# Kernel optimization log

Hardware: AMD Instinct MI355X
Metric: run time of the kernel (lower is better)

Reference implementation:

```python
import jax, jax.numpy as jnp
import numpy as np

DIM = 1024
NUM_HEADS = 16
NUM_KV_HEADS = 4
HEAD_DIM = DIM // NUM_HEADS  # 64
GROUP = NUM_HEADS // NUM_KV_HEADS  # 4
SCALE = HEAD_DIM ** -0.5


def setup_inputs() -> dict:
    key = jax.random.key(0)
    ks = jax.random.split(key, 6)
    B, N = 2, 2048
    x = jax.random.normal(ks[0], (B, N, DIM), dtype=jnp.float32)
    s = DIM ** -0.5
    Wq = jax.random.normal(ks[1], (DIM, DIM), dtype=jnp.float32) * s
    Wk = jax.random.normal(ks[2], (DIM, NUM_KV_HEADS * HEAD_DIM), dtype=jnp.float32) * s
    Wv = jax.random.normal(ks[3], (DIM, NUM_KV_HEADS * HEAD_DIM), dtype=jnp.float32) * s
    Wo = jax.random.normal(ks[4], (DIM, DIM), dtype=jnp.float32) * s
    bo = jax.random.normal(ks[5], (DIM,), dtype=jnp.float32) * 0.01
    return {"x": x, "Wq": Wq, "Wk": Wk, "Wv": Wv, "Wo": Wo, "bo": bo}


def reference(x, Wq, Wk, Wv, Wo, bo):
    B, N, C = x.shape
    # projections
    q = (x @ Wq).reshape(B, N, NUM_HEADS, HEAD_DIM)          # B N H D
    k = (x @ Wk).reshape(B, N, NUM_KV_HEADS, HEAD_DIM)       # B N Kh D
    v = (x @ Wv).reshape(B, N, NUM_KV_HEADS, HEAD_DIM)
    # group query heads: H = Kh * GROUP; broadcast KV per group (no repeat copy)
    q = q.reshape(B, N, NUM_KV_HEADS, GROUP, HEAD_DIM)
    # scores: B Kh G Nq Nk
    attn = jnp.einsum('bqhgd,bkhd->bhgqk', q, k) * SCALE
    attn = jax.nn.softmax(attn, axis=-1)
    out = jnp.einsum('bhgqk,bkhd->bqhgd', attn, v)           # B N Kh G D
    out = out.reshape(B, N, C)
    return out @ Wo + bo
```

## Files before the change

### kernel.cpp

```cpp
#include <hip/hip_runtime.h>
#include <hip/hip_bf16.h>


typedef unsigned short u16;
typedef short s8 __attribute__((ext_vector_type(8)));
typedef float f4 __attribute__((ext_vector_type(4)));
typedef u16 u16x8 __attribute__((ext_vector_type(8)));

__device__ __forceinline__ unsigned pk2(float a, float b) {
  __hip_bfloat162 h = __float22bfloat162_rn(make_float2(a, b));
  unsigned u; __builtin_memcpy(&u, &h, 4); return u;
}
__device__ __forceinline__ u16 bf1(float a) {
  __hip_bfloat16 h = __float2bfloat16(a);
  u16 u; __builtin_memcpy(&u, &h, 2); return u;
}
__device__ __forceinline__ float ex2(float x) {
#if __has_builtin(__builtin_amdgcn_exp2f)
  return __builtin_amdgcn_exp2f(x);
#else
  return exp2f(x);
#endif
}
__device__ __forceinline__ void glds16(const u16* g, u16* l) {
  __builtin_amdgcn_global_load_lds((const __attribute__((address_space(1))) unsigned*)g,
                                   (__attribute__((address_space(3))) unsigned*)l, 16, 0, 0);
}

__global__ __launch_bounds__(256) void cvt_x(const float* __restrict__ x, u16* __restrict__ xb) {
  const int n4 = (4096 * 1024) / 4;
  for (int i = blockIdx.x * 256 + threadIdx.x; i < n4; i += gridDim.x * 256) {
    float4 f = ((const float4*)x)[i];
    uint2 o; o.x = pk2(f.x, f.y); o.y = pk2(f.z, f.w);
    ((uint2*)xb)[i] = o;
  }
}

__global__ __launch_bounds__(256) void cvt_w(const float* __restrict__ Wq, const float* __restrict__ Wk,
                                             const float* __restrict__ Wv, const float* __restrict__ Wo,
                                             u16* __restrict__ wqkvt, u16* __restrict__ wot) {
  __shared__ u16 T[64][68];
  const int m = blockIdx.z;
  const float* src; u16* dst; int N; int drow0; float scale;
  if (m == 0)      { src = Wq; N = 1024; dst = wqkvt; drow0 = 0;    scale = 0.18033688011112042f; }
  else if (m == 1) { src = Wk; N = 256;  dst = wqkvt; drow0 = 1024; scale = 1.f; }
  else if (m == 2) { src = Wv; N = 256;  dst = wqkvt; drow0 = 1280; scale = 1.f; }
  else             { src = Wo; N = 1024; dst = wot;   drow0 = 0;    scale = 1.f; }
  const int n0 = blockIdx.x * 64, k0 = blockIdx.y * 64;
  if (n0 >= N) return;
  const int tid = threadIdx.x;
  const int rr = tid >> 4, cc = (tid & 15) * 4;
#pragma unroll
  for (int it = 0; it < 4; ++it) {
    const int r = rr + it * 16;
    float4 f = *(const float4*)&src[(k0 + r) * N + n0 + cc];
    uint2 o; o.x = pk2(f.x * scale, f.y * scale); o.y = pk2(f.z * scale, f.w * scale);
    *(uint2*)&T[r][cc] = o;
  }
  __syncthreads();
  const int nn = tid >> 3, kq = (tid & 7) * 8;
#pragma unroll
  for (int it = 0; it < 2; ++it) {
    const int n = nn + it * 32;
    u16x8 v;
#pragma unroll
    for (int j = 0; j < 8; ++j) v[j] = T[kq + j][n];
    *(u16x8*)&dst[(drow0 + n0 + n) * 1024 + k0 + kq] = v;
  }
}

__global__ __launch_bounds__(256) void vtrans(const u16* __restrict__ vc, u16* __restrict__ vt) {
  __shared__ u16 T[64][72];
  const int tok0 = blockIdx.x * 64, d0 = blockIdx.y * 64, b = blockIdx.z;
  const int tid = threadIdx.x;
  const int r = tid >> 3, cc = (tid & 7) * 8;
#pragma unroll
  for (int it = 0; it < 2; ++it) {
    const int row = r + it * 32;
    *(u16x8*)&T[row][cc] = *(const u16x8*)&vc[(b * 2048 + tok0 + row) * 256 + d0 + cc];
  }
  __syncthreads();
#pragma unroll
  for (int it = 0; it < 2; ++it) {
    const int d = (tid >> 3) + it * 32;
    const int gd = d0 + d, kh = gd >> 6, dd = gd & 63;
    u16x8 v;
#pragma unroll
    for (int j = 0; j < 8; ++j) v[j] = T[(tid & 7) * 8 + j][d];
    *(u16x8*)&vt[((b * 4 + kh) * 64 + dd) * 2048 + tok0 + (tid & 7) * 8] = v;
  }
}

template<int MODE>
__global__ __launch_bounds__(256) void gemm_bt(const u16* __restrict__ A, const u16* __restrict__ Bt,
                                               u16* __restrict__ Cq, u16* __restrict__ Vc,
                                               float* __restrict__ Cf, const float* __restrict__ bias,
                                               const int K) {
  __shared__ u16 As[128 * 32];
  __shared__ u16 Bs[128 * 32];
  const int tid = threadIdx.x, lane = tid & 63, w = tid >> 6;
  const int wm = w >> 1, wn = w & 1;
  const int m0 = blockIdx.y * 128, n0 = blockIdx.x * 128;
  const int g = lane >> 4, c = lane & 15;
  const int srow = w * 32 + (lane >> 2), scol = (lane & 3) * 8;
  const u16* ga = A + (m0 + srow) * K + scol;
  const u16* gb = Bt + (n0 + srow) * K + scol;
  f4 acc[4][4] = {};
  for (int k0 = 0; k0 < K; k0 += 32) {
    glds16(ga,           &As[w * 1024]);
    glds16(ga + 16 * K,  &As[w * 1024 + 512]);
    glds16(gb,           &Bs[w * 1024]);
    glds16(gb + 16 * K,  &Bs[w * 1024 + 512]);
    ga += 32; gb += 32;
    __syncthreads();
    s8 a[4], b[4];
#pragma unroll
    for (int m = 0; m < 4; ++m) a[m] = *(const s8*)&As[(wm * 64 + m * 16 + c) * 32 + g * 8];
#pragma unroll
    for (int n = 0; n < 4; ++n) b[n] = *(const s8*)&Bs[(wn * 64 + n * 16 + c) * 32 + g * 8];
    __builtin_amdgcn_s_setprio(1);
#pragma unroll
    for (int m = 0; m < 4; ++m)
#pragma unroll
      for (int n = 0; n < 4; ++n)
        acc[m][n] = __builtin_amdgcn_mfma_f32_16x16x32_bf16(a[m], b[n], acc[m][n], 0, 0, 0);
    __builtin_amdgcn_s_setprio(0);
    __syncthreads();
  }
#pragma unroll
  for (int m = 0; m < 4; ++m) {
#pragma unroll
    for (int n = 0; n < 4; ++n) {
#pragma unroll
      for (int r = 0; r < 4; ++r) {
        const int row = m0 + wm * 64 + m * 16 + g * 4 + r;
        const int col = n0 + wn * 64 + n * 16 + c;
        if (MODE == 0) {
          const u16 hv = bf1(acc[m][n][r]);
          if (col < 1280) Cq[row * 1280 + col] = hv;
          else            Vc[row * 256 + (col - 1280)] = hv;
        } else {
          Cf[row * 1024 + col] = acc[m][n][r] + bias[col];
        }
      }
    }
  }
}

__global__ __launch_bounds__(256) void attn_fwd(const u16* __restrict__ qkv, const u16* __restrict__ vt,
                                                u16* __restrict__ ao) {
  __shared__ u16 QP[64 * 64];
  __shared__ u16 Ks[2][64 * 64];
  __shared__ u16 Vs[2][64 * 64];
  const int tid = threadIdx.x, lane = tid & 63, w = tid >> 6;
  const int h = blockIdx.y, b = blockIdx.z, kh = h >> 2;
  const int q0 = blockIdx.x * 64;
  const int g = lane >> 4, c = lane & 15;
  const int srow = w * 16 + (lane >> 3), sch = lane & 7;

#pragma unroll
  for (int j = 0; j < 2; ++j) {
    const int qq = srow + j * 8;
    const int d0 = (sch ^ (qq & 7)) << 3;
    glds16(qkv + (b * 2048 + q0 + qq) * 1280 + h * 64 + d0, &QP[w * 1024 + j * 512]);
  }
  const int rr0 = srow, rr1 = srow + 8;
  const u16* kg0 = qkv + ((b * 2048 + rr0) * 1280) + 1024 + kh * 64 + ((sch ^ (rr0 & 7)) << 3);
  const u16* kg1 = qkv + ((b * 2048 + rr1) * 1280) + 1024 + kh * 64 + ((sch ^ (rr1 & 7)) << 3);
  const u16* vg0 = vt + ((b * 4 + kh) * 64 + rr0) * 2048 + ((sch ^ (rr0 & 7)) << 3);
  const u16* vg1 = vt + ((b * 4 + kh) * 64 + rr1) * 2048 + ((sch ^ (rr1 & 7)) << 3);
  glds16(kg0, &Ks[0][w * 1024]); glds16(kg1, &Ks[0][w * 1024 + 512]);
  glds16(vg0, &Vs[0][w * 1024]); glds16(vg1, &Vs[0][w * 1024 + 512]);
  __syncthreads();

  s8 qf[2];
  {
    const int q = w * 16 + c;
    qf[0] = *(const s8*)&QP[q * 64 + (((0 + g) ^ (q & 7)) << 3)];
    qf[1] = *(const s8*)&QP[q * 64 + (((4 + g) ^ (q & 7)) << 3)];
  }
  const int kb0 = c * 64 + (((0 + g) ^ (c & 7)) << 3);
  const int kb1 = c * 64 + (((4 + g) ^ (c & 7)) << 3);
  const int pwbase = w * 1024 + c * 64;

  s8 ones;
#pragma unroll
  for (int j = 0; j < 8; ++j) ones[j] = (short)0x3F80;

  f4 acc[4] = {};
  f4 accS = {};
  int cur = 0;

  for (int kt = 0; kt < 32; ++kt) {
    if (kt < 31) {
      kg0 += 64 * 1280; kg1 += 64 * 1280; vg0 += 64; vg1 += 64;
      glds16(kg0, &Ks[cur ^ 1][w * 1024]); glds16(kg1, &Ks[cur ^ 1][w * 1024 + 512]);
      glds16(vg0, &Vs[cur ^ 1][w * 1024]); glds16(vg1, &Vs[cur ^ 1][w * 1024 + 512]);
    }
    f4 s[4];
    __builtin_amdgcn_s_setprio(1);
#pragma unroll
    for (int mf = 0; mf < 4; ++mf) {
      const s8 k0 = *(const s8*)&Ks[cur][mf * 1024 + kb0];
      const s8 k1 = *(const s8*)&Ks[cur][mf * 1024 + kb1];
      f4 z = {};
      z = __builtin_amdgcn_mfma_f32_16x16x32_bf16(k0, qf[0], z, 0, 0, 0);
      z = __builtin_amdgcn_mfma_f32_16x16x32_bf16(k1, qf[1], z, 0, 0, 0);
      s[mf] = z;
    }
    __builtin_amdgcn_s_setprio(0);

#pragma unroll
    for (int mf = 0; mf < 4; ++mf) {
      uint2 pk;
      pk.x = pk2(ex2(s[mf][0]), ex2(s[mf][1]));
      pk.y = pk2(ex2(s[mf][2]), ex2(s[mf][3]));
      const int chp = (mf * 2 + (g >> 1)) ^ (c & 7);
      *(uint2*)&QP[pwbase + chp * 8 + (g & 1) * 4] = pk;
    }
    s8 pb[2];
    pb[0] = *(const s8*)&QP[pwbase + (((0 + g) ^ (c & 7)) << 3)];
    pb[1] = *(const s8*)&QP[pwbase + (((4 + g) ^ (c & 7)) << 3)];

    __builtin_amdgcn_s_setprio(1);
#pragma unroll
    for (int df = 0; df < 4; ++df) {
      const s8 v0 = *(const s8*)&Vs[cur][df * 1024 + kb0];
      const s8 v1 = *(const s8*)&Vs[cur][df * 1024 + kb1];
      acc[df] = __builtin_amdgcn_mfma_f32_16x16x32_bf16(v0, pb[0], acc[df], 0, 0, 0);
      acc[df] = __builtin_amdgcn_mfma_f32_16x16x32_bf16(v1, pb[1], acc[df], 0, 0, 0);
    }
    accS = __builtin_amdgcn_mfma_f32_16x16x32_bf16(ones, pb[0], accS, 0, 0, 0);
    accS = __builtin_amdgcn_mfma_f32_16x16x32_bf16(ones, pb[1], accS, 0, 0, 0);
    __builtin_amdgcn_s_setprio(0);
    __syncthreads();
    cur ^= 1;
  }

  const float inv = 1.f / accS[0];
  const int row = b * 2048 + q0 + w * 16 + c;
#pragma unroll
  for (int df = 0; df < 4; ++df) {
    uint2 o; o.x = pk2(acc[df][0] * inv, acc[df][1] * inv);
    o.y = pk2(acc[df][2] * inv, acc[df][3] * inv);
    *(uint2*)&ao[row * 1024 + h * 64 + df * 16 + g * 4] = o;
  }
}

extern "C" void kernel_launch(void* const* d_in, const int* in_sizes, int n_in,
                              void* d_out, int out_size, void* d_ws, size_t ws_size,
                              hipStream_t stream) {
  const float* x  = (const float*)d_in[0];
  const float* Wq = (const float*)d_in[1];
  const float* Wk = (const float*)d_in[2];
  const float* Wv = (const float*)d_in[3];
  const float* Wo = (const float*)d_in[4];
  const float* bo = (const float*)d_in[5];
  float* out = (float*)d_out;

  char* ws = (char*)d_ws;
  u16* xb    = (u16*)(ws);
  u16* ao    = (u16*)(ws);
  u16* wqkvt = (u16*)(ws + 8388608);
  u16* wot   = (u16*)(ws + 11534336);
  u16* qkv   = (u16*)(ws + 13631488);
  u16* vtw   = (u16*)(ws + 24117248);
  u16* vc    = (u16*)(ws + 26214400);

  cvt_x<<<2048, 256, 0, stream>>>(x, xb);
  cvt_w<<<dim3(16, 16, 4), 256, 0, stream>>>(Wq, Wk, Wv, Wo, wqkvt, wot);
  gemm_bt<0><<<dim3(12, 32), 256, 0, stream>>>(xb, wqkvt, qkv, vc, nullptr, nullptr, 1024);
  vtrans<<<dim3(32, 4, 2), 256, 0, stream>>>(vc, vtw);
  attn_fwd<<<dim3(32, 16, 2), 256, 0, stream>>>(qkv, vtw, ao);
  gemm_bt<1><<<dim3(8, 32), 256, 0, stream>>>(ao, wot, nullptr, nullptr, out, bo, 1024);
}
```

Baseline: 196.5 us.

## Split attention keys across warps, fuse conversion kernels, halve GEMM M-tile

Attention now keeps all 64 queries' Q fragments in registers per warp and splits each 128-key tile across the four warps. P goes straight from registers into the PV MFMA with no LDS round-trip, and the partial outputs and denominators are reduced across warps through shared memory at the end. The x and weight conversion kernels are merged into one launch. The GEMMs use 64-row M tiles to double the grid. This removes the per-iteration P store/load and one launch, at the cost of a larger final reduction, more accumulator registers, and less reuse per GEMM tile.

```diff
diff --git a/kernel.cpp b/kernel.cpp
--- a/kernel.cpp
+++ b/kernel.cpp
@@ -4,8 +4,10 @@
 
 typedef unsigned short u16;
 typedef short s8 __attribute__((ext_vector_type(8)));
+typedef short s4 __attribute__((ext_vector_type(4)));
 typedef float f4 __attribute__((ext_vector_type(4)));
 typedef u16 u16x8 __attribute__((ext_vector_type(8)));
+typedef unsigned int u32x4 __attribute__((ext_vector_type(4)));
 
 __device__ __forceinline__ unsigned pk2(float a, float b) {
   __hip_bfloat162 h = __float22bfloat162_rn(make_float2(a, b));
@@ -15,30 +17,28 @@
   __hip_bfloat16 h = __float2bfloat16(a);
   u16 u; __builtin_memcpy(&u, &h, 2); return u;
 }
-__device__ __forceinline__ float ex2(float x) {
-#if __has_builtin(__builtin_amdgcn_exp2f)
-  return __builtin_amdgcn_exp2f(x);
-#else
-  return exp2f(x);
-#endif
-}
+__device__ __forceinline__ float ex2(float x) { return exp2f(x); }
 __device__ __forceinline__ void glds16(const u16* g, u16* l) {
   __builtin_amdgcn_global_load_lds((const __attribute__((address_space(1))) unsigned*)g,
                                    (__attribute__((address_space(3))) unsigned*)l, 16, 0, 0);
 }
 
-__global__ __launch_bounds__(256) void cvt_x(const float* __restrict__ x, u16* __restrict__ xb) {
-  const int n4 = (4096 * 1024) / 4;
-  for (int i = blockIdx.x * 256 + threadIdx.x; i < n4; i += gridDim.x * 256) {
-    float4 f = ((const float4*)x)[i];
-    uint2 o; o.x = pk2(f.x, f.y); o.y = pk2(f.z, f.w);
-    ((uint2*)xb)[i] = o;
-  }
-}
-
-__global__ __launch_bounds__(256) void cvt_w(const float* __restrict__ Wq, const float* __restrict__ Wk,
-                                             const float* __restrict__ Wv, const float* __restrict__ Wo,
-                                             u16* __restrict__ wqkvt, u16* __restrict__ wot) {
+__global__ __launch_bounds__(256) void cvt_all(const float* __restrict__ x,
+                                               const float* __restrict__ Wq, const float* __restrict__ Wk,
+                                               const float* __restrict__ Wv, const float* __restrict__ Wo,
+                                               u16* __restrict__ xb, u16* __restrict__ wqkvt,
+                                               u16* __restrict__ wot) {
+  if (blockIdx.z == 4) {
+    const int base = (blockIdx.y * 16 + blockIdx.x) * 256 + threadIdx.x;
+#pragma unroll
+    for (int j = 0; j < 16; ++j) {
+      const int i = base + j * 65536;
+      float4 f = ((const float4*)x)[i];
+      uint2 o; o.x = pk2(f.x, f.y); o.y = pk2(f.z, f.w);
+      ((uint2*)xb)[i] = o;
+    }
+    return;
+  }
   __shared__ u16 T[64][68];
   const int m = blockIdx.z;
   const float* src; u16* dst; int N; int drow0; float scale;
@@ -96,44 +96,43 @@
                                                u16* __restrict__ Cq, u16* __restrict__ Vc,
                                                float* __restrict__ Cf, const float* __restrict__ bias,
                                                const int K) {
-  __shared__ u16 As[128 * 32];
+  __shared__ u16 As[64 * 32];
   __shared__ u16 Bs[128 * 32];
   const int tid = threadIdx.x, lane = tid & 63, w = tid >> 6;
   const int wm = w >> 1, wn = w & 1;
-  const int m0 = blockIdx.y * 128, n0 = blockIdx.x * 128;
+  const int m0 = blockIdx.y * 64, n0 = blockIdx.x * 128;
   const int g = lane >> 4, c = lane & 15;
-  const int srow = w * 32 + (lane >> 2), scol = (lane & 3) * 8;
-  const u16* ga = A + (m0 + srow) * K + scol;
-  const u16* gb = Bt + (n0 + srow) * K + scol;
-  f4 acc[4][4] = {};
+  const int l2 = lane >> 2, ch = (lane & 3) * 8;
+  const u16* ga = A + (m0 + w * 16 + l2) * K + ch;
+  const u16* gb = Bt + (n0 + w * 32 + l2) * K + ch;
+  f4 acc[2][4] = {};
   for (int k0 = 0; k0 < K; k0 += 32) {
-    glds16(ga,           &As[w * 1024]);
-    glds16(ga + 16 * K,  &As[w * 1024 + 512]);
+    glds16(ga,           &As[w * 512]);
     glds16(gb,           &Bs[w * 1024]);
     glds16(gb + 16 * K,  &Bs[w * 1024 + 512]);
     ga += 32; gb += 32;
     __syncthreads();
-    s8 a[4], b[4];
-#pragma unroll
-    for (int m = 0; m < 4; ++m) a[m] = *(const s8*)&As[(wm * 64 + m * 16 + c) * 32 + g * 8];
-#pragma unroll
-    for (int n = 0; n < 4; ++n) b[n] = *(const s8*)&Bs[(wn * 64 + n * 16 + c) * 32 + g * 8];
+    s8 a[2], b2[4];
+#pragma unroll
+    for (int m = 0; m < 2; ++m) a[m] = *(const s8*)&As[(wm * 32 + m * 16 + c) * 32 + g * 8];
+#pragma unroll
+    for (int n = 0; n < 4; ++n) b2[n] = *(const s8*)&Bs[(wn * 64 + n * 16 + c) * 32 + g * 8];
     __builtin_amdgcn_s_setprio(1);
 #pragma unroll
-    for (int m = 0; m < 4; ++m)
+    for (int m = 0; m < 2; ++m)
 #pragma unroll
       for (int n = 0; n < 4; ++n)
-        acc[m][n] = __builtin_amdgcn_mfma_f32_16x16x32_bf16(a[m], b[n], acc[m][n], 0, 0, 0);
+        acc[m][n] = __builtin_amdgcn_mfma_f32_16x16x32_bf16(a[m], b2[n], acc[m][n], 0, 0, 0);
     __builtin_amdgcn_s_setprio(0);
     __syncthreads();
   }
 #pragma unroll
-  for (int m = 0; m < 4; ++m) {
+  for (int m = 0; m < 2; ++m) {
 #pragma unroll
     for (int n = 0; n < 4; ++n) {
 #pragma unroll
       for (int r = 0; r < 4; ++r) {
-        const int row = m0 + wm * 64 + m * 16 + g * 4 + r;
+        const int row = m0 + wm * 32 + m * 16 + g * 4 + r;
         const int col = n0 + wn * 64 + n * 16 + c;
         if (MODE == 0) {
           const u16 hv = bf1(acc[m][n][r]);
@@ -147,103 +146,129 @@
   }
 }
 
-__global__ __launch_bounds__(256) void attn_fwd(const u16* __restrict__ qkv, const u16* __restrict__ vt,
-                                                u16* __restrict__ ao) {
-  __shared__ u16 QP[64 * 64];
-  __shared__ u16 Ks[2][64 * 64];
-  __shared__ u16 Vs[2][64 * 64];
+__global__ __launch_bounds__(256, 2) void attn_fwd(const u16* __restrict__ qkv,
+                                                   const u16* __restrict__ vt,
+                                                   u16* __restrict__ ao) {
+  __shared__ u16 SMEM[32768];
   const int tid = threadIdx.x, lane = tid & 63, w = tid >> 6;
   const int h = blockIdx.y, b = blockIdx.z, kh = h >> 2;
   const int q0 = blockIdx.x * 64;
   const int g = lane >> 4, c = lane & 15;
-  const int srow = w * 16 + (lane >> 3), sch = lane & 7;
-
-#pragma unroll
-  for (int j = 0; j < 2; ++j) {
-    const int qq = srow + j * 8;
-    const int d0 = (sch ^ (qq & 7)) << 3;
-    glds16(qkv + (b * 2048 + q0 + qq) * 1280 + h * 64 + d0, &QP[w * 1024 + j * 512]);
-  }
-  const int rr0 = srow, rr1 = srow + 8;
-  const u16* kg0 = qkv + ((b * 2048 + rr0) * 1280) + 1024 + kh * 64 + ((sch ^ (rr0 & 7)) << 3);
-  const u16* kg1 = qkv + ((b * 2048 + rr1) * 1280) + 1024 + kh * 64 + ((sch ^ (rr1 & 7)) << 3);
-  const u16* vg0 = vt + ((b * 4 + kh) * 64 + rr0) * 2048 + ((sch ^ (rr0 & 7)) << 3);
-  const u16* vg1 = vt + ((b * 4 + kh) * 64 + rr1) * 2048 + ((sch ^ (rr1 & 7)) << 3);
-  glds16(kg0, &Ks[0][w * 1024]); glds16(kg1, &Ks[0][w * 1024 + 512]);
-  glds16(vg0, &Vs[0][w * 1024]); glds16(vg1, &Vs[0][w * 1024 + 512]);
-  __syncthreads();
-
-  s8 qf[2];
-  {
-    const int q = w * 16 + c;
-    qf[0] = *(const s8*)&QP[q * 64 + (((0 + g) ^ (q & 7)) << 3)];
-    qf[1] = *(const s8*)&QP[q * 64 + (((4 + g) ^ (q & 7)) << 3)];
-  }
-  const int kb0 = c * 64 + (((0 + g) ^ (c & 7)) << 3);
-  const int kb1 = c * 64 + (((4 + g) ^ (c & 7)) << 3);
-  const int pwbase = w * 1024 + c * 64;
+  const int l3 = lane >> 3, ch8 = lane & 7;
+  const int l4 = lane >> 4, ch16 = lane & 15;
+
+  const u16* kgb = qkv + (b * 2048) * 1280 + 1024 + kh * 64;
+  const u16* vgb = vt + ((b * 4 + kh) * 64) * 2048;
+
+  s8 qf[4][2];
+#pragma unroll
+  for (int qb = 0; qb < 4; ++qb) {
+    const u16* qr = qkv + (b * 2048 + q0 + qb * 16 + c) * 1280 + h * 64;
+    qf[qb][0] = *(const s8*)&qr[g * 8];
+    qf[qb][1] = *(const s8*)&qr[32 + g * 8];
+  }
+
+  auto stageKV = [&](int it, int bo) {
+#pragma unroll
+    for (int i = 0; i < 4; ++i) {
+      const int kr = w * 32 + i * 8 + l3;
+      glds16(kgb + (it * 128 + kr) * 1280 + ((ch8 ^ (kr & 7)) << 3),
+             &SMEM[bo + (w * 32 + i * 8) * 64]);
+    }
+#pragma unroll
+    for (int i = 0; i < 4; ++i) {
+      const int vd = w * 16 + i * 4 + l4;
+      glds16(vgb + vd * 2048 + it * 128 + ((ch16 ^ (vd & 7)) << 3),
+             &SMEM[16384 + bo + (w * 16 + i * 4) * 128]);
+    }
+  };
+
+  stageKV(0, 0);
+  __syncthreads();
 
   s8 ones;
 #pragma unroll
   for (int j = 0; j < 8; ++j) ones[j] = (short)0x3F80;
 
-  f4 acc[4] = {};
-  f4 accS = {};
-  int cur = 0;
-
-  for (int kt = 0; kt < 32; ++kt) {
-    if (kt < 31) {
-      kg0 += 64 * 1280; kg1 += 64 * 1280; vg0 += 64; vg1 += 64;
-      glds16(kg0, &Ks[cur ^ 1][w * 1024]); glds16(kg1, &Ks[cur ^ 1][w * 1024 + 512]);
-      glds16(vg0, &Vs[cur ^ 1][w * 1024]); glds16(vg1, &Vs[cur ^ 1][w * 1024 + 512]);
-    }
-    f4 s[4];
+  f4 acc[4][4] = {};
+  f4 accS[4] = {};
+  int bo = 0;
+
+  for (int it = 0; it < 16; ++it) {
+    if (it < 15) stageKV(it + 1, bo ^ 8192);
+
+    s8 kf[2][2];
+#pragma unroll
+    for (int mf = 0; mf < 2; ++mf) {
+      const int krow = bo + (w * 32 + mf * 16 + c) * 64;
+      kf[mf][0] = *(const s8*)&SMEM[krow + ((g ^ (c & 7)) << 3)];
+      kf[mf][1] = *(const s8*)&SMEM[krow + (((4 + g) ^ (c & 7)) << 3)];
+    }
+    s8 vf[4];
+#pragma unroll
+    for (int df = 0; df < 4; ++df) {
+      const int drow = 16384 + bo + (df * 16 + c) * 128;
+      const int cw = c & 7;
+      s4 v0 = *(const s4*)&SMEM[drow + (((w * 4 + (g >> 1)) ^ cw) << 3) + (g & 1) * 4];
+      s4 v1 = *(const s4*)&SMEM[drow + (((w * 4 + 2 + (g >> 1)) ^ cw) << 3) + (g & 1) * 4];
+      vf[df] = __builtin_shufflevector(v0, v1, 0, 1, 2, 3, 4, 5, 6, 7);
+    }
+
     __builtin_amdgcn_s_setprio(1);
 #pragma unroll
-    for (int mf = 0; mf < 4; ++mf) {
-      const s8 k0 = *(const s8*)&Ks[cur][mf * 1024 + kb0];
-      const s8 k1 = *(const s8*)&Ks[cur][mf * 1024 + kb1];
-      f4 z = {};
-      z = __builtin_amdgcn_mfma_f32_16x16x32_bf16(k0, qf[0], z, 0, 0, 0);
-      z = __builtin_amdgcn_mfma_f32_16x16x32_bf16(k1, qf[1], z, 0, 0, 0);
-      s[mf] = z;
-    }
-    __builtin_amdgcn_s_setprio(0);
-
-#pragma unroll
-    for (int mf = 0; mf < 4; ++mf) {
-      uint2 pk;
-      pk.x = pk2(ex2(s[mf][0]), ex2(s[mf][1]));
-      pk.y = pk2(ex2(s[mf][2]), ex2(s[mf][3]));
-      const int chp = (mf * 2 + (g >> 1)) ^ (c & 7);
-      *(uint2*)&QP[pwbase + chp * 8 + (g & 1) * 4] = pk;
-    }
-    s8 pb[2];
-    pb[0] = *(const s8*)&QP[pwbase + (((0 + g) ^ (c & 7)) << 3)];
-    pb[1] = *(const s8*)&QP[pwbase + (((4 + g) ^ (c & 7)) << 3)];
-
-    __builtin_amdgcn_s_setprio(1);
-#pragma unroll
-    for (int df = 0; df < 4; ++df) {
-      const s8 v0 = *(const s8*)&Vs[cur][df * 1024 + kb0];
-      const s8 v1 = *(const s8*)&Vs[cur][df * 1024 + kb1];
-      acc[df] = __builtin_amdgcn_mfma_f32_16x16x32_bf16(v0, pb[0], acc[df], 0, 0, 0);
-      acc[df] = __builtin_amdgcn_mfma_f32_16x16x32_bf16(v1, pb[1], acc[df], 0, 0, 0);
-    }
-    accS = __builtin_amdgcn_mfma_f32_16x16x32_bf16(ones, pb[0], accS, 0, 0, 0);
-    accS = __builtin_amdgcn_mfma_f32_16x16x32_bf16(ones, pb[1], accS, 0, 0, 0);
+    for (int qb = 0; qb < 4; ++qb) {
+      f4 s0 = {}, s1 = {};
+      s0 = __builtin_amdgcn_mfma_f32_16x16x32_bf16(kf[0][0], qf[qb][0], s0, 0, 0, 0);
+      s0 = __builtin_amdgcn_mfma_f32_16x16x32_bf16(kf[0][1], qf[qb][1], s0, 0, 0, 0);
+      s1 = __builtin_amdgcn_mfma_f32_16x16x32_bf16(kf[1][0], qf[qb][0], s1, 0, 0, 0);
+      s1 = __builtin_amdgcn_mfma_f32_16x16x32_bf16(kf[1][1], qf[qb][1], s1, 0, 0, 0);
+      u32x4 pw;
+      pw.x = pk2(ex2(s0[0]), ex2(s0[1]));
+      pw.y = pk2(ex2(s0[2]), ex2(s0[3]));
+      pw.z = pk2(ex2(s1[0]), ex2(s1[1]));
+      pw.w = pk2(ex2(s1[2]), ex2(s1[3]));
+      s8 pb; __builtin_memcpy(&pb, &pw, 16);
+      accS[qb] = __builtin_amdgcn_mfma_f32_16x16x32_bf16(ones, pb, accS[qb], 0, 0, 0);
+#pragma unroll
+      for (int df = 0; df < 4; ++df)
+        acc[df][qb] = __builtin_amdgcn_mfma_f32_16x16x32_bf16(vf[df], pb, acc[df][qb], 0, 0, 0);
+    }
     __builtin_amdgcn_s_setprio(0);
     __syncthreads();
-    cur ^= 1;
-  }
-
-  const float inv = 1.f / accS[0];
-  const int row = b * 2048 + q0 + w * 16 + c;
-#pragma unroll
-  for (int df = 0; df < 4; ++df) {
-    uint2 o; o.x = pk2(acc[df][0] * inv, acc[df][1] * inv);
-    o.y = pk2(acc[df][2] * inv, acc[df][3] * inv);
-    *(uint2*)&ao[row * 1024 + h * 64 + df * 16 + g * 4] = o;
+    bo ^= 8192;
+  }
+
+  float* red = (float*)SMEM;
+#pragma unroll
+  for (int df = 0; df < 4; ++df)
+#pragma unroll
+    for (int qb = 0; qb < 4; ++qb)
+      *(f4*)&red[(w * 16 + df * 4 + qb) * 256 + lane * 4] = acc[df][qb];
+  __syncthreads();
+  f4 sum[4];
+#pragma unroll
+  for (int qb = 0; qb < 4; ++qb) {
+    f4 t = {};
+#pragma unroll
+    for (int j = 0; j < 4; ++j)
+      t += *(const f4*)&red[(j * 16 + w * 4 + qb) * 256 + lane * 4];
+    sum[qb] = t;
+  }
+  __syncthreads();
+  float* sden = (float*)SMEM;
+#pragma unroll
+  for (int qb = 0; qb < 4; ++qb) sden[(w * 4 + qb) * 64 + lane] = accS[qb][0];
+  __syncthreads();
+#pragma unroll
+  for (int qb = 0; qb < 4; ++qb) {
+    float den = 0.f;
+#pragma unroll
+    for (int j = 0; j < 4; ++j) den += sden[(j * 4 + qb) * 64 + lane];
+    const float inv = 1.f / den;
+    uint2 o;
+    o.x = pk2(sum[qb][0] * inv, sum[qb][1] * inv);
+    o.y = pk2(sum[qb][2] * inv, sum[qb][3] * inv);
+    *(uint2*)&ao[(b * 2048 + q0 + qb * 16 + c) * 1024 + h * 64 + w * 16 + g * 4] = o;
   }
 }
 
@@ -267,10 +292,9 @@
   u16* vtw   = (u16*)(ws + 24117248);
   u16* vc    = (u16*)(ws + 26214400);
 
-  cvt_x<<<2048, 256, 0, stream>>>(x, xb);
-  cvt_w<<<dim3(16, 16, 4), 256, 0, stream>>>(Wq, Wk, Wv, Wo, wqkvt, wot);
-  gemm_bt<0><<<dim3(12, 32), 256, 0, stream>>>(xb, wqkvt, qkv, vc, nullptr, nullptr, 1024);
+  cvt_all<<<dim3(16, 16, 5), 256, 0, stream>>>(x, Wq, Wk, Wv, Wo, xb, wqkvt, wot);
+  gemm_bt<0><<<dim3(12, 64), 256, 0, stream>>>(xb, wqkvt, qkv, vc, nullptr, nullptr, 1024);
   vtrans<<<dim3(32, 4, 2), 256, 0, stream>>>(vc, vtw);
   attn_fwd<<<dim3(32, 16, 2), 256, 0, stream>>>(qkv, vtw, ao);
-  gemm_bt<1><<<dim3(8, 32), 256, 0, stream>>>(ao, wot, nullptr, nullptr, out, bo, 1024);
-}
+  gemm_bt<1><<<dim3(8, 64), 256, 0, stream>>>(ao, wot, nullptr, nullptr, out, bo, 1024);
+}
```

New measurement: 193.5 us. Within noise of the previous version (-1.5%).
